# Kernel tuning notes

Measured on AMD Instinct MI355X. Metric: run time of the kernel, lower is better.

The kernel has to match this reference:

```python
import jax, jax.numpy as jnp
import numpy as np
from jax import lax

RADIUS = 4
SIGMA_1 = 5.0
SIGMA_2 = 1.0


def _gaussian_kernel_3d(radius, sigma):
    x = np.linspace(-radius, radius, 2 * radius + 1)
    xx, yy, zz = np.meshgrid(x, x, x)
    dist2 = xx ** 2 + yy ** 2 + zz ** 2
    k = np.exp(-dist2 / (2.0 * sigma ** 2)).astype(np.float32)
    return jnp.asarray(k)[None, None]  # [O=1, I=1, D, H, W]


def _conv3d_same(x, kernel, radius):
    # x: [B,1,D,H,W], kernel: [1,1,kd,kh,kw]
    pad = [(radius, radius)] * 3
    return lax.conv_general_dilated(
        x, kernel, window_strides=(1, 1, 1), padding=pad,
        dimension_numbers=('NCDHW', 'OIDHW', 'NCDHW'))


def setup_inputs() -> dict:
    key = jax.random.key(0)
    k1, k2 = jax.random.split(key)
    labels = jax.random.uniform(k1, (4, 1, 160, 160, 160), dtype=jnp.float32)
    inputs = jax.random.uniform(k2, (4, 1, 160, 160, 160), dtype=jnp.float32)
    return {"labels": labels, "inputs": inputs}


def reference(labels, inputs):
    kernel = _gaussian_kernel_3d(RADIUS, SIGMA_1)
    num_classes = 2
    p0 = labels[:, 0:1]  # [B,1,D,H,W]
    loss = jnp.float32(0.0)
    for k in range(num_classes):
        class_probs = p0 if k == 0 else 1.0 - p0
        class_mean = (jnp.mean(inputs * class_probs, axis=(2, 3, 4), keepdims=True)
                      / (jnp.mean(class_probs, axis=(2, 3, 4), keepdims=True) + 1e-5))
        diff = jnp.sum((inputs - class_mean) ** 2, axis=1, keepdims=True)  # [B,1,D,H,W]
        weights = jnp.exp(-(diff ** 2) / (SIGMA_2 ** 2))
        numerator = jnp.sum(class_probs * _conv3d_same(class_probs * weights, kernel, RADIUS))
        denominator = jnp.sum(class_probs * _conv3d_same(weights, kernel, RADIUS))
        # L1Loss(scalar, 0) == abs(scalar)
        loss = loss + jnp.abs(numerator / (denominator + 1e-6))
    return jnp.float32(num_classes) - loss
```

## Files before the change

kernel.cpp:

```cpp
#include <hip/hip_runtime.h>
#include <hip/hip_fp16.h>
#include <math.h>

#define NX   160
#define N2   25600
#define N3   4096000
#define NB   4

#define ZPB  2
#define NBLK_XY 8000
#define BLKS_PER_B 2000

#define ZCH  10
#define NBLK_Z 1600

#define SB_W 36
#define SB_PLANE (40 * SB_W)

__device__ inline int xcd_swz(int bid, int nblk) {
    return (bid & 7) * (nblk >> 3) + (bid >> 3);
}

__device__ __constant__ float G1[9] = {
    0.72614903f, 0.83527021f, 0.92311635f, 0.98019867f, 1.0f,
    0.98019867f, 0.92311635f, 0.83527021f, 0.72614903f};

#define ES_FULL 7.92946852f
__device__ __constant__ float ES_M[4] = {3.46473426f, 2.48453559f, 1.56141924f,
                                         0.72614903f};
__device__ inline float edge_sum(int i) {
    float s = ES_FULL;
    if (i < 4) s -= ES_M[i];
    if (i > NX - 5) s -= ES_M[NX - 1 - i];
    return s;
}

__device__ inline float4 f4_zero() { return make_float4(0.f, 0.f, 0.f, 0.f); }
__device__ inline float4 f4_axpy(float a, float4 b, float4 c) {
    return make_float4(c.x + a * b.x, c.y + a * b.y, c.z + a * b.z, c.w + a * b.w);
}

__device__ inline float4 load_t4(const __half* p) {
    uint2 u = *(const uint2*)p;
    __half2 a = *(const __half2*)&u.x;
    __half2 b = *(const __half2*)&u.y;
    float2 fa = __half22float2(a);
    float2 fb = __half22float2(b);
    return make_float4(fa.x, fa.y, fb.x, fb.y);
}

template <int NV>
__device__ inline void block_reduce_store(double* vals, double* dst) {
    __shared__ double red[4][NV];
    int lane = threadIdx.x & 63;
    int wave = threadIdx.x >> 6;
#pragma unroll
    for (int v = 0; v < NV; ++v) {
        double x = vals[v];
#pragma unroll
        for (int off = 32; off > 0; off >>= 1) x += __shfl_down(x, off, 64);
        if (lane == 0) red[wave][v] = x;
    }
    __syncthreads();
    if (threadIdx.x < NV) {
        int v = threadIdx.x;
        dst[v] = red[0][v] + red[1][v] + red[2][v] + red[3][v];
    }
}

__global__ __launch_bounds__(256) void conv_xy_kernel(
    const float* __restrict__ labels, const float* __restrict__ inputs,
    __half* __restrict__ t, double* __restrict__ pS) {
    __shared__ float sB[ZPB * SB_PLANE];

    int bid = xcd_swz(blockIdx.x, NBLK_XY);
    int tileX = bid % 5;
    int tileY = (bid / 5) % 5;
    int zq = (bid / 25) % 80;
    int b = bid / BLKS_PER_B;
    int zbase = zq * ZPB;
    int x0 = tileX * 32, y0 = tileY * 32;
    int tid = threadIdx.x;
    int baseOff = b * N3 + zbase * N2;

    for (int i = tid; i < ZPB * 320; i += 256) {
        int j = i / 320;
        int rem = i - 320 * j;
        int r = rem >> 3, x4 = rem & 7;
        int gy = y0 + r - 4;
        int gxf = x0 + 4 * x4 - 4;
        float w[12];
        if (gy >= 0 && gy < NX) {
            const float* row = &labels[baseOff + j * N2 + gy * NX];
#pragma unroll
            for (int c = 0; c < 3; ++c) {
                int gx = gxf + 4 * c;
                float4 v = (gx >= 0 && gx <= NX - 4) ? *(const float4*)&row[gx]
                                                     : f4_zero();
                w[4 * c] = v.x; w[4 * c + 1] = v.y;
                w[4 * c + 2] = v.z; w[4 * c + 3] = v.w;
            }
        } else {
#pragma unroll
            for (int c = 0; c < 12; ++c) w[c] = 0.f;
        }
        float4 o = f4_zero();
#pragma unroll
        for (int d = 0; d < 9; ++d) {
            float g = G1[d];
            o.x += g * w[d];
            o.y += g * w[d + 1];
            o.z += g * w[d + 2];
            o.w += g * w[d + 3];
        }
        *(float4*)&sB[j * SB_PLANE + r * SB_W + 4 * x4] = o;
    }
    __syncthreads();

    int oy = tid >> 3, x4 = tid & 7;
    double sp = 0.0, sip = 0.0, si = 0.0;
#pragma unroll
    for (int j = 0; j < ZPB; ++j) {
        float4 acc = f4_zero();
#pragma unroll
        for (int d = 0; d < 9; ++d) {
            float4 v = *(const float4*)&sB[j * SB_PLANE + (oy + d) * SB_W + 4 * x4];
            acc = f4_axpy(G1[d], v, acc);
        }
        int gi = baseOff + j * N2 + (y0 + oy) * NX + (x0 + 4 * x4);
        __half2 ha = __floats2half2_rn(acc.x, acc.y);
        __half2 hb = __floats2half2_rn(acc.z, acc.w);
        uint2 u;
        u.x = *(unsigned int*)&ha;
        u.y = *(unsigned int*)&hb;
        *(uint2*)&t[gi] = u;

        float4 p = *(const float4*)&labels[gi];
        float4 in = *(const float4*)&inputs[gi];
        sp += (double)(p.x + p.y + p.z + p.w);
        sip += (double)(in.x * p.x + in.y * p.y + in.z * p.z + in.w * p.w);
        si += (double)(in.x + in.y + in.z + in.w);
    }
    double vals[3] = {sp, sip, si};
    block_reduce_store<3>(vals, pS + 3 * bid);
}

__global__ __launch_bounds__(256) void conv_z_kernel(
    const __half* __restrict__ t, const float* __restrict__ labels,
    const float* __restrict__ inputs, const double* __restrict__ pS,
    double* __restrict__ pZ) {
    int tid = threadIdx.x;
    int lbid = xcd_swz(blockIdx.x, NBLK_Z);
    int tidg = lbid * 256 + tid;
    int x4 = tidg % 40;
    int r = tidg / 40;
    int y = r % NX;
    r /= NX;
    int zc = r % 16;
    int b = r / 16;

    __shared__ float sM[2];
    {
        double v0 = 0, v1 = 0, v2 = 0;
        for (int i = tid; i < BLKS_PER_B; i += 256) {
            const double* p = pS + 3 * (b * BLKS_PER_B + i);
            v0 += p[0]; v1 += p[1]; v2 += p[2];
        }
        __shared__ double red[4][3];
        int lane = tid & 63, wave = tid >> 6;
        double vals[3] = {v0, v1, v2};
#pragma unroll
        for (int v = 0; v < 3; ++v) {
            double x = vals[v];
#pragma unroll
            for (int off = 32; off > 0; off >>= 1) x += __shfl_down(x, off, 64);
            if (lane == 0) red[wave][v] = x;
        }
        __syncthreads();
        if (tid == 0) {
            double sp = red[0][0] + red[1][0] + red[2][0] + red[3][0];
            double sip = red[0][1] + red[1][1] + red[2][1] + red[3][1];
            double si = red[0][2] + red[1][2] + red[2][2] + red[3][2];
            const double Nv = (double)N3;
            sM[0] = (float)((sip / Nv) / (sp / Nv + 1e-5));
            sM[1] = (float)(((si - sip) / Nv) / ((Nv - sp) / Nv + 1e-5));
        }
        __syncthreads();
    }
    float m0 = sM[0], m1 = sM[1];

    int x = x4 * 4;
    float ey = edge_sum(y);
    float cx[4] = {edge_sum(x) * ey, edge_sum(x + 1) * ey,
                   edge_sum(x + 2) * ey, edge_sum(x + 3) * ey};

    int z0 = zc * ZCH;
    int base = b * N3 + y * NX + x;

    float4 win[9];
#pragma unroll
    for (int d = 0; d < 9; ++d) {
        int z = z0 - 4 + d;
        win[d] = (z >= 0 && z < NX) ? load_t4(&t[base + z * N2]) : f4_zero();
    }

    float n0 = 0.f, d0 = 0.f, n1 = 0.f, d1 = 0.f;
    for (int zb = 0; zb < 5; ++zb) {
        int z = z0 + 2 * zb;
        float4 tn[2], pv[2], iv[2];
#pragma unroll
        for (int j = 0; j < 2; ++j) {
            int zl = z + j + 5;
            tn[j] = (zl < NX) ? load_t4(&t[base + zl * N2]) : f4_zero();
            int gi = base + (z + j) * N2;
            pv[j] = *(const float4*)&labels[gi];
            iv[j] = *(const float4*)&inputs[gi];
        }
#pragma unroll
        for (int j = 0; j < 2; ++j) {
            float4 c4 = f4_zero();
#pragma unroll
            for (int d = 0; d < 9; ++d) c4 = f4_axpy(G1[d], win[d], c4);
            float ez = edge_sum(z + j);
            float pc[4] = {pv[j].x, pv[j].y, pv[j].z, pv[j].w};
            float ic[4] = {iv[j].x, iv[j].y, iv[j].z, iv[j].w};
            float cc[4] = {c4.x, c4.y, c4.z, c4.w};
#pragma unroll
            for (int l = 0; l < 4; ++l) {
                float c1 = cx[l] * ez - cc[l];
                float df0 = ic[l] - m0; df0 *= df0;
                float w0 = __expf(-df0 * df0);
                float df1 = ic[l] - m1; df1 *= df1;
                float w1 = __expf(-df1 * df1);
                n0 += cc[l] * pc[l] * w0;
                d0 += cc[l] * w0;
                n1 += c1 * (1.f - pc[l]) * w1;
                d1 += c1 * w1;
            }
#pragma unroll
            for (int d = 0; d < 8; ++d) win[d] = win[d + 1];
            win[8] = tn[j];
        }
    }
    double vals[4] = {(double)n0, (double)d0, (double)n1, (double)d1};
    block_reduce_store<4>(vals, pZ + 4 * lbid);
}

__global__ __launch_bounds__(256) void finalize_kernel(
    const double* __restrict__ pZ, float* __restrict__ out) {
    double a0 = 0, a1 = 0, a2 = 0, a3 = 0;
    for (int i = threadIdx.x; i < NBLK_Z; i += 256) {
        const double* p = &pZ[4 * i];
        a0 += p[0]; a1 += p[1]; a2 += p[2]; a3 += p[3];
    }
    __shared__ double red[4][4];
    int lane = threadIdx.x & 63;
    int wave = threadIdx.x >> 6;
    double vals[4] = {a0, a1, a2, a3};
#pragma unroll
    for (int v = 0; v < 4; ++v) {
        double x = vals[v];
#pragma unroll
        for (int off = 32; off > 0; off >>= 1) x += __shfl_down(x, off, 64);
        if (lane == 0) red[wave][v] = x;
    }
    __syncthreads();
    if (threadIdx.x == 0) {
        double acc[4];
#pragma unroll
        for (int v = 0; v < 4; ++v)
            acc[v] = red[0][v] + red[1][v] + red[2][v] + red[3][v];
        double r0 = fabs(acc[0] / (acc[1] + 1e-6));
        double r1 = fabs(acc[2] / (acc[3] + 1e-6));
        out[0] = (float)(2.0 - r0 - r1);
    }
}

extern "C" void kernel_launch(void* const* d_in, const int* in_sizes, int n_in,
                              void* d_out, int out_size, void* d_ws, size_t ws_size,
                              hipStream_t stream) {
    const float* labels = (const float*)d_in[0];
    const float* inputs = (const float*)d_in[1];
    float* out = (float*)d_out;

    double* pS = (double*)d_ws;
    double* pZ = (double*)((char*)d_ws + 192128);
    __half* t  = (__half*)((char*)d_ws + 524288);

    hipLaunchKernelGGL(conv_xy_kernel, dim3(NBLK_XY), dim3(256), 0, stream,
                       labels, inputs, t, pS);
    hipLaunchKernelGGL(conv_z_kernel, dim3(NBLK_Z), dim3(256), 0, stream,
                       t, labels, inputs, pS, pZ);
    hipLaunchKernelGGL(finalize_kernel, dim3(1), dim3(256), 0, stream, pZ, out);
}
```

Before: 202.2 us.

## Replace shared-memory XY tile conv with per-thread sliding register window along Y

The XY separable convolution no longer stages a 40x32 tile in LDS with a block barrier. Each thread now owns a 4-wide x column and walks a 10-row y chunk, keeping a 9-entry register window of x-filtered rows and adding one new row per output. This removes the LDS traffic, the halo recomputation per 32x32 tile and the __syncthreads, at the cost of more registers and fewer blocks (1600 instead of 8000), which shrinks the partial-sum array read by the z kernel.

```diff
diff --git a/kernel.cpp b/kernel.cpp
--- a/kernel.cpp
+++ b/kernel.cpp
@@ -7,15 +7,12 @@
 #define N3   4096000
 #define NB   4
 
-#define ZPB  2
-#define NBLK_XY 8000
-#define BLKS_PER_B 2000
+#define YCH  10
+#define NBLK_XY 1600
+#define XY_BLKS_PER_B 400
 
 #define ZCH  10
 #define NBLK_Z 1600
-
-#define SB_W 36
-#define SB_PLANE (40 * SB_W)
 
 __device__ inline int xcd_swz(int bid, int nblk) {
     return (bid & 7) * (nblk >> 3) + (bid >> 3);
@@ -71,78 +68,91 @@
 __global__ __launch_bounds__(256) void conv_xy_kernel(
     const float* __restrict__ labels, const float* __restrict__ inputs,
     __half* __restrict__ t, double* __restrict__ pS) {
-    __shared__ float sB[ZPB * SB_PLANE];
-
-    int bid = xcd_swz(blockIdx.x, NBLK_XY);
-    int tileX = bid % 5;
-    int tileY = (bid / 5) % 5;
-    int zq = (bid / 25) % 80;
-    int b = bid / BLKS_PER_B;
-    int zbase = zq * ZPB;
-    int x0 = tileX * 32, y0 = tileY * 32;
     int tid = threadIdx.x;
-    int baseOff = b * N3 + zbase * N2;
-
-    for (int i = tid; i < ZPB * 320; i += 256) {
-        int j = i / 320;
-        int rem = i - 320 * j;
-        int r = rem >> 3, x4 = rem & 7;
-        int gy = y0 + r - 4;
-        int gxf = x0 + 4 * x4 - 4;
+    int lbid = xcd_swz(blockIdx.x, NBLK_XY);
+    int tidg = lbid * 256 + tid;
+    int x4 = tidg % 40;
+    int r = tidg / 40;
+    int yc = r % 16;
+    r /= 16;
+    int z = r % NX;
+    int b = r / NX;
+
+    int x0 = x4 * 4;
+    int y0 = yc * YCH;
+    const float* plane = labels + b * N3 + z * N2;
+    const float* iplane = inputs + b * N3 + z * N2;
+    __half* tplane = t + b * N3 + z * N2;
+
+    float4 win[9];
+#pragma unroll
+    for (int d = 0; d < 9; ++d) {
+        int gy = y0 - 4 + d;
+        bool rowok = (gy >= 0) && (gy < NX);
         float w[12];
-        if (gy >= 0 && gy < NX) {
-            const float* row = &labels[baseOff + j * N2 + gy * NX];
-#pragma unroll
-            for (int c = 0; c < 3; ++c) {
-                int gx = gxf + 4 * c;
-                float4 v = (gx >= 0 && gx <= NX - 4) ? *(const float4*)&row[gx]
-                                                     : f4_zero();
-                w[4 * c] = v.x; w[4 * c + 1] = v.y;
-                w[4 * c + 2] = v.z; w[4 * c + 3] = v.w;
-            }
-        } else {
-#pragma unroll
-            for (int c = 0; c < 12; ++c) w[c] = 0.f;
+#pragma unroll
+        for (int c = 0; c < 3; ++c) {
+            int gx = x0 - 4 + 4 * c;
+            float4 v = (rowok && gx >= 0 && gx <= NX - 4)
+                           ? *(const float4*)&plane[gy * NX + gx]
+                           : f4_zero();
+            w[4 * c] = v.x; w[4 * c + 1] = v.y;
+            w[4 * c + 2] = v.z; w[4 * c + 3] = v.w;
         }
         float4 o = f4_zero();
 #pragma unroll
-        for (int d = 0; d < 9; ++d) {
-            float g = G1[d];
-            o.x += g * w[d];
-            o.y += g * w[d + 1];
-            o.z += g * w[d + 2];
-            o.w += g * w[d + 3];
-        }
-        *(float4*)&sB[j * SB_PLANE + r * SB_W + 4 * x4] = o;
-    }
-    __syncthreads();
-
-    int oy = tid >> 3, x4 = tid & 7;
+        for (int k = 0; k < 9; ++k) {
+            float g = G1[k];
+            o.x += g * w[k];     o.y += g * w[k + 1];
+            o.z += g * w[k + 2]; o.w += g * w[k + 3];
+        }
+        win[d] = o;
+    }
+
     double sp = 0.0, sip = 0.0, si = 0.0;
-#pragma unroll
-    for (int j = 0; j < ZPB; ++j) {
+#pragma unroll 2
+    for (int yo = 0; yo < YCH; ++yo) {
+        int y = y0 + yo;
+        int gy = y + 5;
+        bool rowok = (gy < NX) && (yo < YCH - 1);
+        float w[12];
+#pragma unroll
+        for (int c = 0; c < 3; ++c) {
+            int gx = x0 - 4 + 4 * c;
+            float4 v = (rowok && gx >= 0 && gx <= NX - 4)
+                           ? *(const float4*)&plane[gy * NX + gx]
+                           : f4_zero();
+            w[4 * c] = v.x; w[4 * c + 1] = v.y;
+            w[4 * c + 2] = v.z; w[4 * c + 3] = v.w;
+        }
+        int go = y * NX + x0;
+        float4 p = *(const float4*)&plane[go];
+        float4 in = *(const float4*)&iplane[go];
         float4 acc = f4_zero();
 #pragma unroll
-        for (int d = 0; d < 9; ++d) {
-            float4 v = *(const float4*)&sB[j * SB_PLANE + (oy + d) * SB_W + 4 * x4];
-            acc = f4_axpy(G1[d], v, acc);
-        }
-        int gi = baseOff + j * N2 + (y0 + oy) * NX + (x0 + 4 * x4);
+        for (int d = 0; d < 9; ++d) acc = f4_axpy(G1[d], win[d], acc);
         __half2 ha = __floats2half2_rn(acc.x, acc.y);
         __half2 hb = __floats2half2_rn(acc.z, acc.w);
         uint2 u;
         u.x = *(unsigned int*)&ha;
         u.y = *(unsigned int*)&hb;
-        *(uint2*)&t[gi] = u;
-
-        float4 p = *(const float4*)&labels[gi];
-        float4 in = *(const float4*)&inputs[gi];
+        *(uint2*)&tplane[go] = u;
         sp += (double)(p.x + p.y + p.z + p.w);
         sip += (double)(in.x * p.x + in.y * p.y + in.z * p.z + in.w * p.w);
         si += (double)(in.x + in.y + in.z + in.w);
+        float4 o = f4_zero();
+#pragma unroll
+        for (int k = 0; k < 9; ++k) {
+            float g = G1[k];
+            o.x += g * w[k];     o.y += g * w[k + 1];
+            o.z += g * w[k + 2]; o.w += g * w[k + 3];
+        }
+#pragma unroll
+        for (int d = 0; d < 8; ++d) win[d] = win[d + 1];
+        win[8] = o;
     }
     double vals[3] = {sp, sip, si};
-    block_reduce_store<3>(vals, pS + 3 * bid);
+    block_reduce_store<3>(vals, pS + 3 * lbid);
 }
 
 __global__ __launch_bounds__(256) void conv_z_kernel(
@@ -162,8 +172,8 @@
     __shared__ float sM[2];
     {
         double v0 = 0, v1 = 0, v2 = 0;
-        for (int i = tid; i < BLKS_PER_B; i += 256) {
-            const double* p = pS + 3 * (b * BLKS_PER_B + i);
+        for (int i = tid; i < XY_BLKS_PER_B; i += 256) {
+            const double* p = pS + 3 * (b * XY_BLKS_PER_B + i);
             v0 += p[0]; v1 += p[1]; v2 += p[2];
         }
         __shared__ double red[4][3];
```

New measurement: 201.4 us. Within noise of the previous version (-0.4%).
